# Optimization experiments

Measured on AMD Instinct MI355X. Metric: run time of the kernel, lower is better.

## Reference

```python
import jax, jax.numpy as jnp
import numpy as np

M = 256
N = 256
J = 2
L = 4
F = J * L  # number of Morlet wavelets
PI = float(np.pi)


def _make_grid(m, n):
    gm = np.arange(-(m // 2), -(m // 2) + m, dtype=np.float32)
    gn = np.arange(-(n // 2), -(n // 2) + n, dtype=np.float32)
    return jnp.asarray(np.stack(np.meshgrid(gm, gn, indexing='ij'), 0))  # [2, M, N]

GRID = _make_grid(M, N)


def morlet_filters(theta, xis, sigmas, slants, morlet=True):
    """Build Fourier-domain Morlet (or Gabor/Gaussian) filters, [F, M, N] complex64."""
    c, s = jnp.cos(theta), jnp.sin(theta)
    wave_vectors = jnp.stack([c, s], axis=1) * xis[:, None]                   # [F, 2]
    # orthonormal basis per filter: row0 along wave direction, row1 perpendicular
    basis = jnp.stack([jnp.stack([c, s], 1), jnp.stack([-s, c], 1)], axis=1)  # [F, 2, 2]
    gauss_dirs = basis / sigmas[:, None, None]
    slant_mod = jnp.stack([slants, jnp.ones_like(slants)], axis=1)            # [F, 2]
    gauss_dirs = gauss_dirs * slant_mod[:, :, None]
    phase = jnp.einsum('fd,dmn->fmn', wave_vectors, GRID)                     # [F, M, N]
    waves = jnp.exp(1j * phase)
    radii2 = jnp.sum(jnp.einsum('fed,dmn->femn', gauss_dirs, GRID) ** 2, axis=1)
    gauss = jnp.exp(-0.5 * radii2)
    if morlet:
        gs = gauss.sum(axis=(-2, -1), keepdims=True)
        ws = (waves * gauss).sum(axis=(-2, -1), keepdims=True)
        filt = (waves - ws / gs) * gauss  # zero-mean Morlet correction
    else:
        filt = waves * gauss
    norm = (2.0 * PI * sigmas * sigmas / slants)[:, None, None]
    filt = filt / norm
    filt = jnp.fft.ifftshift(filt, axes=(-2, -1))
    return jnp.fft.fft2(filt)


def low_pass_phi():
    # Gaussian low-pass at scale 2**J (xi = 0, Gabor without Morlet correction)
    th = jnp.zeros((1,), jnp.float32)
    xi = jnp.zeros((1,), jnp.float32)
    sg = jnp.full((1,), 0.8 * 2.0 ** J, jnp.float32)
    sl = jnp.ones((1,), jnp.float32)
    return morlet_filters(th, xi, sg, sl, morlet=False)[0]  # [M, N]


def setup_inputs() -> dict:
    key = jax.random.key(0)
    x = jax.random.normal(key, (4, 2, M, N), dtype=jnp.float32)
    # Tight-Frame initialization of the J*L learnable wavelet parameters
    js = np.repeat(np.arange(J), L).astype(np.float32)
    theta = np.tile((int(L - L / 2 - 1) - np.arange(L)) * np.pi / L, J).astype(np.float32)
    xis = (3.0 / 4.0 * np.pi / 2.0 ** js).astype(np.float32)
    sigmas = (0.8 * 2.0 ** js).astype(np.float32)
    slants = np.full(J * L, 4.0 / L, dtype=np.float32)
    return {"x": x, "theta": jnp.asarray(theta), "xis": jnp.asarray(xis),
            "sigmas": jnp.asarray(sigmas), "slants": jnp.asarray(slants)}


def reference(x, theta, xis, sigmas, slants):
    """Order-2 wavelet scattering on periodic fields via FFT conv + modulus.
    Returns [B, (1 + F + F*F) * C, M, N]."""
    B, C = x.shape[0], x.shape[1]
    sub = 1  # subsample factor (module default)
    psi = morlet_filters(theta, xis, sigmas, slants)        # [F, M, N] complex
    phi = low_pass_phi()                                    # [M, N] complex
    Xh = jnp.fft.fft2(x)                                    # [B, C, M, N]
    S0 = jnp.fft.ifft2(Xh * phi).real[:, :, None]           # [B, C, 1, M, N]
    U1 = jnp.abs(jnp.fft.ifft2(Xh[:, :, None] * psi))       # [B, C, F, M, N]
    U1h = jnp.fft.fft2(U1)
    U2 = jnp.abs(jnp.fft.ifft2(U1h[:, :, :, None] * psi))   # [B, C, F, F, M, N]
    S = jnp.concatenate([S0, U1, U2.reshape(B, C, F * F, M, N)], axis=2)
    S = S[..., ::sub, ::sub]
    return S.reshape(B, (1 + F + F * F) * C, M // sub, N // sub)
```

## Files before the change

### kernel.cpp

```cpp
#include <hip/hip_runtime.h>
#include <math.h>

#define PI_F 3.14159265358979323846f
#define IMG 65536
#define RW 4

__device__ __forceinline__ float2 cmul(float2 a, float2 b) {
  return make_float2(a.x * b.x - a.y * b.y, a.x * b.y + a.y * b.x);
}
__device__ __forceinline__ float2 shflx(float2 v, int m) {
  return make_float2(__shfl_xor(v.x, m, 64), __shfl_xor(v.y, m, 64));
}

template <int CTRL>
__device__ __forceinline__ float2 dppx(float2 v) {
  float2 r;
  r.x = __int_as_float(__builtin_amdgcn_update_dpp(
      0, __float_as_int(v.x), CTRL, 0xf, 0xf, true));
  r.y = __int_as_float(__builtin_amdgcn_update_dpp(
      0, __float_as_int(v.y), CTRL, 0xf, 0xf, true));
  return r;
}
__device__ __forceinline__ float2 partner(float2 v, int s) {
  switch (s) {
    case 1: return dppx<0xB1>(v);
    case 2: return dppx<0x4E>(v);
    case 8: return dppx<0x128>(v);
    default: return shflx(v, s);
  }
}

struct Tw { float2 w[5]; float2 q1, q2, q3; };

__device__ __forceinline__ void tw_make(int lane, float sign, Tw& T) {
  #pragma unroll
  for (int t = 0; t < 5; ++t) {
    int s = 32 >> t;
    if (lane & s) {
      float ang = sign * PI_F * (float)(lane & (s - 1)) / (float)s;
      float sn, cs; __sincosf(ang, &sn, &cs);
      T.w[t] = make_float2(cs, sn);
    } else {
      T.w[t] = make_float2(1.f, 0.f);
    }
  }
  float ang = sign * 2.f * PI_F * (float)lane * (1.f / 256.f);
  float sn, cs; __sincosf(ang, &sn, &cs);
  T.q1 = make_float2(cs, sn);
  T.q2 = cmul(T.q1, T.q1);
  T.q3 = cmul(T.q2, T.q1);
}


__device__ __forceinline__ void fwd256_b(float2 (&v)[RW][4], int lane, const Tw& T) {
  #pragma unroll
  for (int r = 0; r < RW; ++r) {
    float2 a = v[r][0], b = v[r][1], c = v[r][2], d = v[r][3];
    float2 e0 = make_float2(a.x + c.x, a.y + c.y);
    float2 o0 = make_float2(a.x - c.x, a.y - c.y);
    float2 e1 = make_float2(b.x + d.x, b.y + d.y);
    float2 o1 = make_float2(b.x - d.x, b.y - d.y);
    v[r][0] = make_float2(e0.x + e1.x, e0.y + e1.y);
    v[r][2] = cmul(make_float2(e0.x - e1.x, e0.y - e1.y), T.q2);
    v[r][1] = cmul(make_float2(o0.x + o1.y, o0.y - o1.x), T.q1);
    v[r][3] = cmul(make_float2(o0.x - o1.y, o0.y + o1.x), T.q3);
  }
  #pragma unroll
  for (int t = 0; t < 5; ++t) {
    int s = 32 >> t;
    float sg = (lane & s) ? -1.f : 1.f;
    float2 w = T.w[t];
    #pragma unroll
    for (int r = 0; r < RW; ++r)
      #pragma unroll
      for (int j = 0; j < 4; ++j) {
        float2 p = partner(v[r][j], s);
        float2 u = make_float2(p.x + sg * v[r][j].x, p.y + sg * v[r][j].y);
        v[r][j] = cmul(u, w);
      }
  }
  {
    float sg = (lane & 1) ? -1.f : 1.f;
    #pragma unroll
    for (int r = 0; r < RW; ++r)
      #pragma unroll
      for (int j = 0; j < 4; ++j) {
        float2 p = partner(v[r][j], 1);
        v[r][j] = make_float2(p.x + sg * v[r][j].x, p.y + sg * v[r][j].y);
      }
  }
}

__device__ __forceinline__ void inv256_b(float2 (&v)[RW][4], int lane, const Tw& T) {
  {
    float sg = (lane & 1) ? -1.f : 1.f;
    #pragma unroll
    for (int r = 0; r < RW; ++r)
      #pragma unroll
      for (int j = 0; j < 4; ++j) {
        float2 p = partner(v[r][j], 1);
        v[r][j] = make_float2(p.x + sg * v[r][j].x, p.y + sg * v[r][j].y);
      }
  }
  #pragma unroll
  for (int t = 0; t < 5; ++t) {
    int s = 2 << t;
    float sg = (lane & s) ? -1.f : 1.f;
    float2 w = T.w[4 - t];
    #pragma unroll
    for (int r = 0; r < RW; ++r)
      #pragma unroll
      for (int j = 0; j < 4; ++j) {
        float2 z = cmul(v[r][j], w);
        float2 p = partner(z, s);
        v[r][j] = make_float2(p.x + sg * z.x, p.y + sg * z.y);
      }
  }
  #pragma unroll
  for (int r = 0; r < RW; ++r) {
    float2 a = v[r][0], b = cmul(v[r][1], T.q1);
    float2 c = cmul(v[r][2], T.q2), d = cmul(v[r][3], T.q3);
    float2 e0 = make_float2(a.x + c.x, a.y + c.y);
    float2 o0 = make_float2(a.x - c.x, a.y - c.y);
    float2 e1 = make_float2(b.x + d.x, b.y + d.y);
    float2 o1 = make_float2(b.x - d.x, b.y - d.y);
    v[r][0] = make_float2(e0.x + e1.x, e0.y + e1.y);
    v[r][2] = make_float2(e0.x - e1.x, e0.y - e1.y);
    v[r][1] = make_float2(o0.x - o1.y, o0.y + o1.x);
    v[r][3] = make_float2(o0.x + o1.y, o0.y - o1.x);
  }
}


__device__ __forceinline__ void loadRows(const float2* bp, int r0, float2 (&v)[RW][4], int l) {
  #pragma unroll
  for (int ri = 0; ri < RW; ++ri) {
    const float2* rp = bp + (size_t)(r0 + ri) * 256 + l;
    #pragma unroll
    for (int j = 0; j < 4; ++j) v[ri][j] = rp[64 * j];
  }
}
__device__ __forceinline__ void storeRows(float2* bp, int r0, float2 (&v)[RW][4], int l) {
  #pragma unroll
  for (int ri = 0; ri < RW; ++ri) {
    float2* rp = bp + (size_t)(r0 + ri) * 256 + l;
    #pragma unroll
    for (int j = 0; j < 4; ++j) rp[64 * j] = v[ri][j];
  }
}

__device__ __forceinline__ void storeT_lds(float2* OT, int R0,
                                           float2 (&v)[RW][4], int w, int l) {
  __shared__ float2 tile[16][256];
  #pragma unroll
  for (int ri = 0; ri < RW; ++ri)
    #pragma unroll
    for (int j = 0; j < 4; ++j)
      tile[w * RW + ri][l + 64 * j] = v[ri][j];
  __syncthreads();
  int c = w * 64 + l;
  float4* dst = (float4*)(OT + (size_t)c * 256 + R0);
  #pragma unroll
  for (int k = 0; k < 8; ++k) {
    float2 a = tile[2 * k][c], b = tile[2 * k + 1][c];
    dst[k] = make_float4(a.x, a.y, b.x, b.y);
  }
}


__global__ __launch_bounds__(256) void k_sums(const float* th, const float* xi,
                                              const float* sg, const float* sl,
                                              float* sums) {
  int f = blockIdx.x, t = threadIdx.x;
  float c, s;
  sincosf(th[f], &s, &c);
  float X = xi[f], S = sg[f], SL = sl[f];
  float a0x = SL * c / S, a0y = SL * s / S, a1x = -s / S, a1y = c / S;
  float gs = 0.f, wr = 0.f, wi = 0.f;
  for (int p = t; p < IMG; p += 256) {
    float gm = (float)((p >> 8) - 128);
    float gn = (float)((p & 255) - 128);
    float r0 = a0x * gm + a0y * gn, r1 = a1x * gm + a1y * gn;
    float g = __expf(-0.5f * (r0 * r0 + r1 * r1));
    float sp, cp;
    sincosf(X * (c * gm + s * gn), &sp, &cp);
    gs += g; wr += cp * g; wi += sp * g;
  }
  __shared__ float red[3][256];
  red[0][t] = gs; red[1][t] = wr; red[2][t] = wi;
  __syncthreads();
  for (int o = 128; o > 0; o >>= 1) {
    if (t < o) {
      red[0][t] += red[0][t + o];
      red[1][t] += red[1][t + o];
      red[2][t] += red[2][t + o];
    }
    __syncthreads();
  }
  if (t == 0) {
    sums[f * 3 + 0] = red[0][0];
    sums[f * 3 + 1] = red[1][0];
    sums[f * 3 + 2] = red[2][0];
  }
}

__global__ __launch_bounds__(256) void k_pre1(const float* __restrict__ x,
                                              const float* th, const float* xi,
                                              const float* sg_, const float* sl,
                                              const float* sums, float2* outT) {
  int w = threadIdx.x >> 6, l = threadIdx.x & 63;
  int y = blockIdx.y;
  int R0 = blockIdx.x * 16;
  int r0 = R0 + w * RW;
  float2 v[RW][4];
  if (y >= 9) {
    int img = y - 9;
    #pragma unroll
    for (int ri = 0; ri < RW; ++ri) {
      const float* rp = x + (size_t)img * IMG + (size_t)(r0 + ri) * 256 + l;
      #pragma unroll
      for (int j = 0; j < 4; ++j) v[ri][j] = make_float2(rp[64 * j], 0.f);
    }
  } else {
    int f = y;
    bool isPhi = (f == 8);
    float T_ = 0.f, X = 0.f, S = 3.2f, SL = 1.f, Kr = 0.f, Ki = 0.f;
    if (!isPhi) {
      T_ = th[f]; X = xi[f]; S = sg_[f]; SL = sl[f];
      float gs = sums[f * 3];
      Kr = sums[f * 3 + 1] / gs;
      Ki = sums[f * 3 + 2] / gs;
    }
    float c, s;
    sincosf(T_, &s, &c);
    float a0x = SL * c / S, a0y = SL * s / S, a1x = -s / S, a1y = c / S;
    float inorm = SL / (2.f * PI_F * S * S);
    #pragma unroll
    for (int ri = 0; ri < RW; ++ri) {
      int m = r0 + ri;
      float gm = (m < 128) ? (float)m : (float)(m - 256);
      #pragma unroll
      for (int j = 0; j < 4; ++j) {
        int n = l + 64 * j;
        float gn = (n < 128) ? (float)n : (float)(n - 256);
        float rr0 = a0x * gm + a0y * gn, rr1 = a1x * gm + a1y * gn;
        float g = __expf(-0.5f * (rr0 * rr0 + rr1 * rr1));
        float sp, cp;
        sincosf(X * (c * gm + s * gn), &sp, &cp);
        float re = isPhi ? g : (cp - Kr) * g;
        float im = isPhi ? 0.f : (sp - Ki) * g;
        v[ri][j] = make_float2(re * inorm, im * inorm);
      }
    }
  }
  Tw T; tw_make(l, -1.f, T);
  fwd256_b(v, l, T);
  storeT_lds(outT + (size_t)y * IMG, R0, v, w, l);
}

__global__ __launch_bounds__(256) void k_fwdS(const float2* in, float2* out) {
  int w = threadIdx.x >> 6, l = threadIdx.x & 63;
  int img = blockIdx.y, r0 = blockIdx.x * 16 + w * RW;
  float2 v[RW][4];
  loadRows(in + (size_t)img * IMG, r0, v, l);
  Tw T; tw_make(l, -1.f, T);
  fwd256_b(v, l, T);
  storeRows(out + (size_t)img * IMG, r0, v, l);
}

__global__ __launch_bounds__(256) void k_u1_p1(const float2* __restrict__ XhT,
                                               const float2* __restrict__ psiT,
                                               float* out) {
  int w = threadIdx.x >> 6, l = threadIdx.x & 63;
  int y = blockIdx.y, i = y / 9, f = y - i * 9;
  int R0 = blockIdx.x * 16;
  int r0 = R0 + w * RW;
  const float2* A = XhT + (size_t)i * IMG;
  const float2* P = psiT + (size_t)f * IMG;
  float2 v[RW][4];
  #pragma unroll
  for (int ri = 0; ri < RW; ++ri) {
    const float2* ap = A + (size_t)(r0 + ri) * 256 + l;
    const float2* pp = P + (size_t)(r0 + ri) * 256 + l;
    #pragma unroll
    for (int j = 0; j < 4; ++j) v[ri][j] = cmul(ap[64 * j], pp[64 * j]);
  }
  Tw T; tw_make(l, 1.f, T);
  inv256_b(v, l, T);
  storeT_lds((float2*)out + ((size_t)(i * 73 + 9 + 2 * f)) * 32768, R0, v, w, l);
}

__global__ __launch_bounds__(256) void k_u1_p2(float* out, float2* T2) {
  int w = threadIdx.x >> 6, l = threadIdx.x & 63;
  int y = blockIdx.y, i = y / 9, f = y - i * 9;
  int R0 = blockIdx.x * 16;
  int r0 = R0 + w * RW;
  float2 v[RW][4];
  loadRows((const float2*)out + ((size_t)(i * 73 + 9 + 2 * f)) * 32768, r0, v, l);
  Tw Ti; tw_make(l, 1.f, Ti);
  inv256_b(v, l, Ti);
  if (f == 8) {
    float* op = out + (size_t)(i * 73) * IMG;
    #pragma unroll
    for (int ri = 0; ri < RW; ++ri)
      #pragma unroll
      for (int j = 0; j < 4; ++j)
        op[(size_t)(r0 + ri) * 256 + l + 64 * j] = v[ri][j].x * (1.f / 65536.f);
    return;
  }
  float* uo = out + (size_t)(i * 73 + 1 + f) * IMG;
  #pragma unroll
  for (int ri = 0; ri < RW; ++ri)
    #pragma unroll
    for (int j = 0; j < 4; ++j) {
      float2 z = v[ri][j];
      float mod = sqrtf(z.x * z.x + z.y * z.y) * (1.f / 65536.f);
      uo[(size_t)(r0 + ri) * 256 + l + 64 * j] = mod;
      v[ri][j] = make_float2(mod, 0.f);
    }
  Tw Tf; tw_make(l, -1.f, Tf);
  fwd256_b(v, l, Tf);
  storeT_lds(T2 + (size_t)(i * 8 + f) * IMG, R0, v, w, l);
}

__global__ __launch_bounds__(256) void k_u2_p1(const float2* __restrict__ U1hT,
                                               const float2* __restrict__ psiT,
                                               float2* __restrict__ T3, int q0) {
  int w = threadIdx.x >> 6, l = threadIdx.x & 63;
  int y = blockIdx.y, q = q0 + (y >> 3), f2 = y & 7;
  int f1 = q >> 3, ii = q & 7;
  int R0 = blockIdx.x * 16;
  int r0 = R0 + w * RW;
  const float2* A = U1hT + (size_t)(ii * 8 + f1) * IMG;
  const float2* P = psiT + (size_t)f2 * IMG;
  float2 v[RW][4];
  #pragma unroll
  for (int ri = 0; ri < RW; ++ri) {
    const float2* ap = A + (size_t)(r0 + ri) * 256 + l;
    const float2* pp = P + (size_t)(r0 + ri) * 256 + l;
    #pragma unroll
    for (int j = 0; j < 4; ++j) v[ri][j] = cmul(ap[64 * j], pp[64 * j]);
  }
  Tw T; tw_make(l, 1.f, T);
  inv256_b(v, l, T);
  storeT_lds(T3 + (size_t)y * IMG, R0, v, w, l);
}

__global__ __launch_bounds__(256) void k_u2_p2(const float2* __restrict__ T3,
                                               float* __restrict__ out, int q0) {
  int w = threadIdx.x >> 6, l = threadIdx.x & 63;
  int y = blockIdx.y, q = q0 + (y >> 3), f2 = y & 7;
  int f1 = q >> 3, ii = q & 7;
  int r0 = blockIdx.x * 16 + w * RW;
  float2 v[RW][4];
  loadRows(T3 + (size_t)y * IMG, r0, v, l);
  Tw T; tw_make(l, 1.f, T);
  inv256_b(v, l, T);
  float* op = out + (size_t)(ii * 73 + 9 + f1 * 8 + f2) * IMG;
  #pragma unroll
  for (int ri = 0; ri < RW; ++ri)
    #pragma unroll
    for (int j = 0; j < 4; ++j) {
      float2 z = v[ri][j];
      op[(size_t)(r0 + ri) * 256 + l + 64 * j] =
          sqrtf(z.x * z.x + z.y * z.y) * (1.f / 65536.f);
    }
}

extern "C" void kernel_launch(void* const* d_in, const int* in_sizes, int n_in,
                              void* d_out, int out_size, void* d_ws, size_t ws_size,
                              hipStream_t stream) {
  const float* x  = (const float*)d_in[0];
  const float* th = (const float*)d_in[1];
  const float* xi = (const float*)d_in[2];
  const float* sg = (const float*)d_in[3];
  const float* sl = (const float*)d_in[4];
  float* out = (float*)d_out;

  float* sums  = (float*)d_ws;
  float2* psiT = (float2*)((char*)d_ws + 1024);
  float2* XhT  = psiT + (size_t)9 * IMG;
  float2* T2   = XhT + (size_t)8 * IMG;
  float2* T3   = T2 + (size_t)64 * IMG;
  float2* tmp17 = T2;

  size_t base = 1024 + (size_t)(9 + 8 + 64) * IMG * sizeof(float2);
  int CQ = 16;
  while (CQ > 1 && base + (size_t)CQ * 8 * IMG * sizeof(float2) > ws_size) CQ >>= 1;

  const int GX = 16;
  dim3 B(256);
  k_sums <<<dim3(8),      B, 0, stream>>>(th, xi, sg, sl, sums);
  k_pre1 <<<dim3(GX, 17), B, 0, stream>>>(x, th, xi, sg, sl, sums, tmp17);
  k_fwdS <<<dim3(GX, 17), B, 0, stream>>>(tmp17, psiT);
  k_u1_p1<<<dim3(GX, 72), B, 0, stream>>>(XhT, psiT, out);
  k_u1_p2<<<dim3(GX, 72), B, 0, stream>>>(out, T2);
  k_fwdS <<<dim3(GX, 64), B, 0, stream>>>(T2, T2);
  for (int q0 = 0; q0 < 64; q0 += CQ) {
    k_u2_p1<<<dim3(GX, CQ * 8), B, 0, stream>>>(T2, psiT, T3, q0);
    k_u2_p2<<<dim3(GX, CQ * 8), B, 0, stream>>>(T3, out, q0);
  }
}
```

Before: 483.8 us.

## Fuse second-stage forward FFT into U2 pass and reuse it across all f2 filters

Removes the separate k_fwdS launch over the 64 U1 images. The row FFT of each U1 image is now done inside k_u2_p1f, held in registers, and multiplied by all 8 psi filters in a loop. Each filter product is then inverse-transformed and stored. This cuts global reads of U1hT eightfold and drops a full-image pass. In exchange each block does 8 times more serial work, the grid has 8 times fewer blocks, and the workspace chunk grows to CQ=64, which means fewer but larger launches and a bigger T3 buffer.

```diff
diff --git a/kernel.cpp b/kernel.cpp
--- a/kernel.cpp
+++ b/kernel.cpp
@@ -49,6 +49,11 @@
   T.q1 = make_float2(cs, sn);
   T.q2 = cmul(T.q1, T.q1);
   T.q3 = cmul(T.q2, T.q1);
+}
+__device__ __forceinline__ void tw_conj(Tw& T) {
+  #pragma unroll
+  for (int t = 0; t < 5; ++t) T.w[t].y = -T.w[t].y;
+  T.q1.y = -T.q1.y; T.q2.y = -T.q2.y; T.q3.y = -T.q3.y;
 }
 
 
@@ -323,27 +328,34 @@
   storeT_lds(T2 + (size_t)(i * 8 + f) * IMG, R0, v, w, l);
 }
 
-__global__ __launch_bounds__(256) void k_u2_p1(const float2* __restrict__ U1hT,
-                                               const float2* __restrict__ psiT,
-                                               float2* __restrict__ T3, int q0) {
-  int w = threadIdx.x >> 6, l = threadIdx.x & 63;
-  int y = blockIdx.y, q = q0 + (y >> 3), f2 = y & 7;
+__global__ __launch_bounds__(256) void k_u2_p1f(const float2* __restrict__ T2,
+                                                const float2* __restrict__ psiT,
+                                                float2* __restrict__ T3, int q0) {
+  int w = threadIdx.x >> 6, l = threadIdx.x & 63;
+  int qi = blockIdx.y, q = q0 + qi;
   int f1 = q >> 3, ii = q & 7;
   int R0 = blockIdx.x * 16;
   int r0 = R0 + w * RW;
-  const float2* A = U1hT + (size_t)(ii * 8 + f1) * IMG;
-  const float2* P = psiT + (size_t)f2 * IMG;
-  float2 v[RW][4];
-  #pragma unroll
-  for (int ri = 0; ri < RW; ++ri) {
-    const float2* ap = A + (size_t)(r0 + ri) * 256 + l;
-    const float2* pp = P + (size_t)(r0 + ri) * 256 + l;
-    #pragma unroll
-    for (int j = 0; j < 4; ++j) v[ri][j] = cmul(ap[64 * j], pp[64 * j]);
-  }
-  Tw T; tw_make(l, 1.f, T);
-  inv256_b(v, l, T);
-  storeT_lds(T3 + (size_t)y * IMG, R0, v, w, l);
+  const float2* A = T2 + (size_t)(ii * 8 + f1) * IMG;
+  float2 a[RW][4];
+  loadRows(A, r0, a, l);
+  Tw T; tw_make(l, -1.f, T);
+  fwd256_b(a, l, T);
+  tw_conj(T);
+  #pragma unroll 1
+  for (int f2 = 0; f2 < 8; ++f2) {
+    const float2* P = psiT + (size_t)f2 * IMG;
+    float2 v[RW][4];
+    #pragma unroll
+    for (int ri = 0; ri < RW; ++ri) {
+      const float2* pp = P + (size_t)(r0 + ri) * 256 + l;
+      #pragma unroll
+      for (int j = 0; j < 4; ++j) v[ri][j] = cmul(a[ri][j], pp[64 * j]);
+    }
+    inv256_b(v, l, T);
+    __syncthreads();
+    storeT_lds(T3 + (size_t)(qi * 8 + f2) * IMG, R0, v, w, l);
+  }
 }
 
 __global__ __launch_bounds__(256) void k_u2_p2(const float2* __restrict__ T3,
@@ -385,7 +397,7 @@
   float2* tmp17 = T2;
 
   size_t base = 1024 + (size_t)(9 + 8 + 64) * IMG * sizeof(float2);
-  int CQ = 16;
+  int CQ = 64;
   while (CQ > 1 && base + (size_t)CQ * 8 * IMG * sizeof(float2) > ws_size) CQ >>= 1;
 
   const int GX = 16;
@@ -395,9 +407,8 @@
   k_fwdS <<<dim3(GX, 17), B, 0, stream>>>(tmp17, psiT);
   k_u1_p1<<<dim3(GX, 72), B, 0, stream>>>(XhT, psiT, out);
   k_u1_p2<<<dim3(GX, 72), B, 0, stream>>>(out, T2);
-  k_fwdS <<<dim3(GX, 64), B, 0, stream>>>(T2, T2);
   for (int q0 = 0; q0 < 64; q0 += CQ) {
-    k_u2_p1<<<dim3(GX, CQ * 8), B, 0, stream>>>(T2, psiT, T3, q0);
-    k_u2_p2<<<dim3(GX, CQ * 8), B, 0, stream>>>(T3, out, q0);
-  }
-}
+    k_u2_p1f<<<dim3(GX, CQ),     B, 0, stream>>>(T2, psiT, T3, q0);
+    k_u2_p2 <<<dim3(GX, CQ * 8), B, 0, stream>>>(T3, out, q0);
+  }
+}
```

Result: slower. 529.8 us (+9.5%).
